# Kernel tuning notes

Measured on AMD Instinct MI355X. Metric: run time of the kernel, lower is better.

The kernel has to match this reference:

```python
import jax, jax.numpy as jnp
import numpy as np

N = 50000
E = 800000
F_IN = 128
HEADS = 8
HID = 16
CLASSES = 40
NEG_SLOPE = 0.2


def setup_inputs() -> dict:
    key = jax.random.key(0)
    ks = jax.random.split(key, 10)
    return {
        "x": jax.random.normal(ks[0], (N, F_IN), jnp.float32),
        "edge_index": jax.random.randint(ks[1], (2, E), 0, N, jnp.int64),
        "W1": jax.random.normal(ks[2], (F_IN, HEADS * HID), jnp.float32) * 0.1,
        "a_src1": jax.random.normal(ks[3], (HEADS, HID), jnp.float32) * 0.1,
        "a_dst1": jax.random.normal(ks[4], (HEADS, HID), jnp.float32) * 0.1,
        "b1": jax.random.normal(ks[5], (HEADS * HID,), jnp.float32) * 0.1,
        "W2": jax.random.normal(ks[6], (HEADS * HID, CLASSES), jnp.float32) * 0.1,
        "a_src2": jax.random.normal(ks[7], (1, CLASSES), jnp.float32) * 0.1,
        "a_dst2": jax.random.normal(ks[8], (1, CLASSES), jnp.float32) * 0.1,
        "b2": jax.random.normal(ks[9], (CLASSES,), jnp.float32) * 0.1,
    }


def gat_conv(x, src, dst, W, a_src, a_dst, bias, heads, out_ch, concat):
    # x: [N, in] -> h: [N, H, C]
    h = (x @ W).reshape(N, heads, out_ch)
    e_src = jnp.einsum("nhc,hc->nh", h, a_src)  # [N, H]
    e_dst = jnp.einsum("nhc,hc->nh", h, a_dst)
    alpha = e_src[src] + e_dst[dst]             # [E, H]
    alpha = jax.nn.leaky_relu(alpha, NEG_SLOPE)
    # segment softmax over incoming edges of each dst node
    amax = jax.ops.segment_max(alpha, dst, num_segments=N)
    alpha = jnp.exp(alpha - amax[dst])
    denom = jax.ops.segment_sum(alpha, dst, num_segments=N)
    alpha = alpha / (denom[dst] + 1e-16)
    msg = h[src] * alpha[:, :, None]            # [E, H, C]
    out = jax.ops.segment_sum(msg, dst, num_segments=N)  # [N, H, C]
    out = out.reshape(N, heads * out_ch) if concat else out.mean(axis=1)
    return out + bias


def reference(x, edge_index, W1, a_src1, a_dst1, b1, W2, a_src2, a_dst2, b2):
    # PyG GATConv adds self-loops by default
    loops = jnp.arange(N, dtype=edge_index.dtype)
    src = jnp.concatenate([edge_index[0], loops])
    dst = jnp.concatenate([edge_index[1], loops])
    # inference: dropout layers are identity
    h = gat_conv(x, src, dst, W1, a_src1, a_dst1, b1, HEADS, HID, concat=True)
    h = jax.nn.elu(h)
    out = gat_conv(h, src, dst, W2, a_src2, a_dst2, b2, 1, CLASSES, concat=False)
    return out
```

## Files before the change

kernel.cpp:

```cpp
#include <hip/hip_runtime.h>
#include <math.h>

#define NN 50000
#define EE 800000
#define ET (EE + NN)
#define F_IN 128
#define HEADS 8
#define HID 16
#define C1 (HEADS * HID)
#define CLASSES 40
#define NEG_SLOPE 0.2f
#define LOG2E 1.4426950408889634f

#define NCHUNKS ((NN + 1023) / 1024)
#define NHIST 64
#define EPB (EE / NHIST)
#define PADN (NCHUNKS * 1024)
#define LDSW (PADN / 4)
#define GB ((NN + 63) / 64)

typedef __attribute__((ext_vector_type(8))) short bf16x8;
typedef __attribute__((ext_vector_type(4))) float f32x4;
typedef __attribute__((ext_vector_type(8))) _Float16 h16x8;
typedef __attribute__((ext_vector_type(2))) _Float16 h16x2;

__device__ __forceinline__ unsigned cvtpk(float a, float b) {
    unsigned r;
    asm("v_cvt_pk_bf16_f32 %0, %1, %2" : "=v"(r) : "v"(a), "v"(b));
    return r;
}
__device__ __forceinline__ float fexp2(float x) {
    float r;
    asm("v_exp_f32 %0, %1\n\ts_nop 0" : "=v"(r) : "v"(x));
    return r;
}
__device__ __forceinline__ float bflo(unsigned u) { return __uint_as_float(u << 16); }
__device__ __forceinline__ float bfhi(unsigned u) { return __uint_as_float(u & 0xffff0000u); }
__device__ __forceinline__ float lrelu(float a) { return fmaxf(a, NEG_SLOPE * a); }
__device__ __forceinline__ unsigned short bf1(float a) { return (unsigned short)cvtpk(a, a); }
__device__ __forceinline__ float bf1f(float a) { return bflo(cvtpk(a, a)); }
__device__ __forceinline__ bf16x8 pack8(float f0, float f1, float f2, float f3,
                                        float f4, float f5, float f6, float f7) {
    union { unsigned u[4]; bf16x8 v; } U;
    U.u[0] = cvtpk(f0, f1);
    U.u[1] = cvtpk(f2, f3);
    U.u[2] = cvtpk(f4, f5);
    U.u[3] = cvtpk(f6, f7);
    return U.v;
}

__global__ void prep_kernel(const float* __restrict__ W1,
                            const float* __restrict__ as1, const float* __restrict__ ad1,
                            const float* __restrict__ W2,
                            const float* __restrict__ as2, const float* __restrict__ ad2,
                            const int* __restrict__ ei,
                            unsigned short* __restrict__ va1h, unsigned short* __restrict__ va1l,
                            unsigned short* __restrict__ va2b,
                            unsigned short* __restrict__ W1b, unsigned short* __restrict__ W2b,
                            unsigned char* __restrict__ partial8,
                            unsigned char* __restrict__ rank8) {
    const int tid = threadIdx.x;
    const int b = blockIdx.x;
    if (b >= 3) {
        __shared__ unsigned lhist[LDSW];
        for (int i = tid; i < LDSW; i += 256) lhist[i] = 0;
        __syncthreads();
        const int hb = b - 3;
        const int* dp = ei + EE + hb * EPB;
        unsigned char* rk = rank8 + (size_t)hb * EPB;
        for (int e0 = tid * 4; e0 < EPB; e0 += 1024) {
            int4 d4 = *(const int4*)(dp + e0);
            uchar4 r;
            {
                const unsigned d = (unsigned)d4.x, sh8 = (d & 3) << 3;
                unsigned old = atomicAdd(&lhist[d >> 2], 1u << sh8);
                r.x = (unsigned char)((old >> sh8) & 0xff);
            }
            {
                const unsigned d = (unsigned)d4.y, sh8 = (d & 3) << 3;
                unsigned old = atomicAdd(&lhist[d >> 2], 1u << sh8);
                r.y = (unsigned char)((old >> sh8) & 0xff);
            }
            {
                const unsigned d = (unsigned)d4.z, sh8 = (d & 3) << 3;
                unsigned old = atomicAdd(&lhist[d >> 2], 1u << sh8);
                r.z = (unsigned char)((old >> sh8) & 0xff);
            }
            {
                const unsigned d = (unsigned)d4.w, sh8 = (d & 3) << 3;
                unsigned old = atomicAdd(&lhist[d >> 2], 1u << sh8);
                r.w = (unsigned char)((old >> sh8) & 0xff);
            }
            *(uchar4*)(rk + e0) = r;
        }
        __syncthreads();
        unsigned* pb = (unsigned*)(partial8 + (size_t)hb * PADN);
        for (int i = tid; i < LDSW; i += 256) pb[i] = lhist[i];
        return;
    }
    if (b == 1) {
        for (int f = tid; f < 2048; f += 256) {
            const int lane = f & 63, kc = (f >> 6) & 3, ntw = f >> 8;
            const int q = lane >> 4, c = lane & 15;
            const int col = ntw * 16 + c;
            const int k0 = kc * 32 + q * 8;
            const float* wp = W1 + (size_t)k0 * C1 + col;
            *(bf16x8*)(W1b + (size_t)f * 8) =
                pack8(wp[0], wp[C1], wp[2 * C1], wp[3 * C1],
                      wp[4 * C1], wp[5 * C1], wp[6 * C1], wp[7 * C1]);
        }
        return;
    }
    if (b == 2) {
        for (int f = tid; f < 768; f += 256) {
            const int lane = f & 63, kc = (f >> 6) & 3, nt = f >> 8;
            const int q = lane >> 4, c = lane & 15;
            const int col = nt * 16 + c;
            const int k0 = kc * 32 + q * 8;
            bf16x8 v = 0;
            if (col < CLASSES) {
                const float* wp = W2 + (size_t)k0 * CLASSES + col;
                v = pack8(wp[0], wp[CLASSES], wp[2 * CLASSES], wp[3 * CLASSES],
                          wp[4 * CLASSES], wp[5 * CLASSES], wp[6 * CLASSES], wp[7 * CLASSES]);
            }
            *(bf16x8*)(W2b + (size_t)f * 8) = v;
        }
        return;
    }
    {
        const int k = tid >> 1, half = tid & 1;
        const float* wrow = W1 + (size_t)k * C1 + half * 64;
        #pragma unroll
        for (int hh = 0; hh < 4; ++hh) {
            const int h = half * 4 + hh;
            float s = 0.f, d = 0.f;
            #pragma unroll
            for (int t = 0; t < 16; ++t) {
                float wv = wrow[hh * 16 + t];
                s += wv * as1[h * HID + t];
                d += wv * ad1[h * HID + t];
            }
            s *= LOG2E; d *= LOG2E;
            va1h[h * 128 + k]       = bf1(s);
            va1l[h * 128 + k]       = bf1(s - bf1f(s));
            va1h[(h + 8) * 128 + k] = bf1(d);
            va1l[(h + 8) * 128 + k] = bf1(d - bf1f(d));
        }
    }
    if (tid < C1) {
        const float* wrow = W2 + (size_t)tid * CLASSES;
        float s = 0.f, d = 0.f;
        #pragma unroll
        for (int c2 = 0; c2 < CLASSES; ++c2) {
            float wv = wrow[c2];
            s += wv * as2[c2];
            d += wv * ad2[c2];
        }
        s *= LOG2E; d *= LOG2E;
        va2b[0 * 128 + tid] = bf1(s);
        va2b[1 * 128 + tid] = bf1(s - bf1f(s));
        va2b[2 * 128 + tid] = bf1(d);
        va2b[3 * 128 + tid] = bf1(d - bf1f(d));
    }
}

__global__ void scan1_kernel(const unsigned char* __restrict__ partial8,
                             unsigned char* __restrict__ pfx8,
                             int* __restrict__ deg,
                             int* __restrict__ rowptr, int* __restrict__ bsum) {
    __shared__ int sh[256];
    const int tid = threadIdx.x;
    const int base = blockIdx.x * 1024 + tid * 4;
    int t0 = 0, t1 = 0, t2 = 0, t3 = 0;
    #pragma unroll 8
    for (int b = 0; b < NHIST; ++b) {
        uchar4 pf;
        pf.x = (unsigned char)t0; pf.y = (unsigned char)t1;
        pf.z = (unsigned char)t2; pf.w = (unsigned char)t3;
        *(uchar4*)(pfx8 + (size_t)b * PADN + base) = pf;
        uchar4 p = *(const uchar4*)(partial8 + (size_t)b * PADN + base);
        t0 += p.x; t1 += p.y; t2 += p.z; t3 += p.w;
    }
    int v[4], s[4];
    v[0] = (base + 0 < NN) ? t0 + 1 : 0;
    v[1] = (base + 1 < NN) ? t1 + 1 : 0;
    v[2] = (base + 2 < NN) ? t2 + 1 : 0;
    v[3] = (base + 3 < NN) ? t3 + 1 : 0;
    #pragma unroll
    for (int j = 0; j < 4; ++j)
        if (base + j < NN) deg[base + j] = v[j];
    s[0] = v[0]; s[1] = s[0] + v[1]; s[2] = s[1] + v[2]; s[3] = s[2] + v[3];
    int T = s[3];
    sh[tid] = T;
    __syncthreads();
    for (int off = 1; off < 256; off <<= 1) {
        int xv = (tid >= off) ? sh[tid - off] : 0;
        __syncthreads();
        sh[tid] += xv;
        __syncthreads();
    }
    int excl = sh[tid] - T;
    #pragma unroll
    for (int j = 0; j < 4; ++j)
        if (base + j < NN) rowptr[base + j] = excl + s[j] - v[j];
    if (tid == 255) bsum[blockIdx.x] = sh[255];
}

__global__ void scan3_kernel(int* __restrict__ rowptr, const int* __restrict__ bsum,
                             unsigned short* __restrict__ csr) {
    __shared__ int ex[64];
    const int tid = threadIdx.x;
    if (tid < 64) {
        int v = (tid < NCHUNKS) ? bsum[tid] : 0;
        int s = v;
        #pragma unroll
        for (int off = 1; off < 64; off <<= 1) {
            int xv = __shfl_up(s, off);
            if (tid >= off) s += xv;
        }
        ex[tid] = s - v;
    }
    __syncthreads();
    int i = blockIdx.x * blockDim.x + tid;
    if (i >= NN) return;
    int rp = rowptr[i] + ex[i >> 10];
    rowptr[i] = rp;
    csr[rp] = (unsigned short)i;
}

__global__ __launch_bounds__(256, 4)
void gemm1_fill_kernel(const float* __restrict__ x,
                       const unsigned short* __restrict__ W1b,
                       const unsigned short* __restrict__ va1h,
                       const unsigned short* __restrict__ va1l,
                       const int* __restrict__ ei,
                       const int* __restrict__ rowptr,
                       const unsigned char* __restrict__ pfx8,
                       const unsigned char* __restrict__ rank8,
                       unsigned short* __restrict__ csr,
                       _Float16* __restrict__ h1h,
                       float* __restrict__ e_src, float* __restrict__ e_dst) {
    const int bid = blockIdx.x;
    const int tid = threadIdx.x;
    if (bid < NHIST) {
        const int fb = bid;
        const int* sp = ei + fb * EPB;
        const int* dp = ei + EE + fb * EPB;
        const unsigned char* pf = pfx8 + (size_t)fb * PADN;
        const unsigned char* rk = rank8 + (size_t)fb * EPB;
        for (int e0 = tid * 4; e0 < EPB; e0 += 1024) {
            int4 s4 = *(const int4*)(sp + e0);
            int4 d4 = *(const int4*)(dp + e0);
            uchar4 r = *(const uchar4*)(rk + e0);
            csr[rowptr[d4.x] + 1 + pf[d4.x] + r.x] = (unsigned short)s4.x;
            csr[rowptr[d4.y] + 1 + pf[d4.y] + r.y] = (unsigned short)s4.y;
            csr[rowptr[d4.z] + 1 + pf[d4.z] + r.z] = (unsigned short)s4.z;
            csr[rowptr[d4.w] + 1 + pf[d4.w] + r.w] = (unsigned short)s4.w;
        }
        return;
    }
    const int gemmb = bid - NHIST;
    const int w = tid >> 6, lane = tid & 63;
    const int q = lane >> 4, c = lane & 15;
    const int m0 = (gemmb * 4 + w) * 16;

    int row = m0 + c;
    if (row > NN - 1) row = NN - 1;
    bf16x8 afrag[4];
    #pragma unroll
    for (int kc = 0; kc < 4; ++kc) {
        const float* xp = x + (size_t)row * F_IN + kc * 32 + q * 8;
        float4 p0 = *(const float4*)xp;
        float4 p1 = *(const float4*)(xp + 4);
        afrag[kc] = pack8(p0.x, p0.y, p0.z, p0.w, p1.x, p1.y, p1.z, p1.w);
    }

    {
        f32x4 acce = {0.f, 0.f, 0.f, 0.f};
        #pragma unroll
        for (int kc = 0; kc < 4; ++kc) {
            const int coloff = kc * 32 + q * 8;
            bf16x8 beh = *(const bf16x8*)(va1h + c * 128 + coloff);
            bf16x8 bel = *(const bf16x8*)(va1l + c * 128 + coloff);
            acce = __builtin_amdgcn_mfma_f32_16x16x32_bf16(afrag[kc], beh, acce, 0, 0, 0);
            acce = __builtin_amdgcn_mfma_f32_16x16x32_bf16(afrag[kc], bel, acce, 0, 0, 0);
        }
        float* ep = (c < 8) ? e_src : e_dst;
        const int cc = c & 7;
        #pragma unroll
        for (int r = 0; r < 4; ++r) {
            const int ro = m0 + q * 4 + r;
            if (ro < NN) ep[(size_t)ro * HEADS + cc] = acce[r];
        }
    }

    #pragma unroll 2
    for (int nt = 0; nt < 8; ++nt) {
        bf16x8 bf0 = *(const bf16x8*)(W1b + (size_t)((nt * 4 + 0) * 64 + lane) * 8);
        bf16x8 bf1_ = *(const bf16x8*)(W1b + (size_t)((nt * 4 + 1) * 64 + lane) * 8);
        bf16x8 bf2 = *(const bf16x8*)(W1b + (size_t)((nt * 4 + 2) * 64 + lane) * 8);
        bf16x8 bf3 = *(const bf16x8*)(W1b + (size_t)((nt * 4 + 3) * 64 + lane) * 8);
        f32x4 a = {0.f, 0.f, 0.f, 0.f};
        a = __builtin_amdgcn_mfma_f32_16x16x32_bf16(afrag[0], bf0, a, 0, 0, 0);
        a = __builtin_amdgcn_mfma_f32_16x16x32_bf16(afrag[1], bf1_, a, 0, 0, 0);
        a = __builtin_amdgcn_mfma_f32_16x16x32_bf16(afrag[2], bf2, a, 0, 0, 0);
        a = __builtin_amdgcn_mfma_f32_16x16x32_bf16(afrag[3], bf3, a, 0, 0, 0);
        #pragma unroll
        for (int r = 0; r < 4; ++r) {
            const int ro = m0 + q * 4 + r;
            if (ro < NN) h1h[(size_t)ro * C1 + nt * 16 + c] = (_Float16)a[r];
        }
    }
}

__global__ __launch_bounds__(64)
void agg1_kernel(const _Float16* __restrict__ h1h,
                 const float* __restrict__ e_src, const float* __restrict__ e_dst,
                 const int* __restrict__ rowptr, const int* __restrict__ deg,
                 const unsigned short* __restrict__ csr,
                 const float* __restrict__ b1, unsigned short* __restrict__ hmid) {
    const int tid = threadIdx.x;
    const int l = tid & 15;
    const int d = blockIdx.x * 4 + (tid >> 4);
    const int hd = l >> 1;
    const float ed = e_dst[(size_t)d * HEADS + hd];
    const int start = rowptr[d];
    const int cnt = deg[d];

    float denom = 0.f;
    float acc[8] = {0.f, 0.f, 0.f, 0.f, 0.f, 0.f, 0.f, 0.f};

    for (int i = 0; i < cnt; i += 8) {
        int s[8];
        #pragma unroll
        for (int e = 0; e < 8; ++e)
            s[e] = csr[start + ((i + e < cnt) ? i + e : i)];
        float es[8];
        #pragma unroll
        for (int e = 0; e < 8; ++e)
            es[e] = e_src[(size_t)s[e] * HEADS + hd];
        h16x8 g[8];
        #pragma unroll
        for (int e = 0; e < 8; ++e)
            g[e] = *(const h16x8*)(h1h + (size_t)s[e] * C1 + 8 * l);
        float w[8];
        #pragma unroll
        for (int e = 0; e < 8; ++e) {
            float we = fexp2(lrelu(es[e] + ed));
            w[e] = (i + e < cnt) ? we : 0.f;
            denom += w[e];
        }
        #pragma unroll
        for (int e = 0; e < 8; ++e) {
            #pragma unroll
            for (int j = 0; j < 8; ++j)
                acc[j] = fmaf((float)g[e][j], w[e], acc[j]);
        }
    }
    const float inv = 1.f / (denom + 1e-16f);
    float o[8];
    #pragma unroll
    for (int k = 0; k < 8; ++k) {
        float t = acc[k] * inv + b1[8 * l + k];
        o[k] = (t > 0.f) ? t : fexp2(t * LOG2E) - 1.f;
    }
    uint4 st;
    st.x = cvtpk(o[0], o[1]);
    st.y = cvtpk(o[2], o[3]);
    st.z = cvtpk(o[4], o[5]);
    st.w = cvtpk(o[6], o[7]);
    *(uint4*)(hmid + (size_t)d * C1 + 8 * l) = st;
}

__global__ __launch_bounds__(256, 4)
void gemm2_kernel(const unsigned short* __restrict__ hmid,
                  const unsigned short* __restrict__ W2b,
                  const unsigned short* __restrict__ va2b,
                  _Float16* __restrict__ h2h,
                  float* __restrict__ e_src, float* __restrict__ e_dst) {
    const int tid = threadIdx.x;
    const int w = tid >> 6, lane = tid & 63;
    const int q = lane >> 4, c = lane & 15;

    const int m0 = (blockIdx.x * 4 + w) * 16;
    if (m0 >= NN) return;
    int row = m0 + c;
    if (row > NN - 1) row = NN - 1;
    bf16x8 afrag[4];
    #pragma unroll
    for (int kc = 0; kc < 4; ++kc)
        afrag[kc] = *(const bf16x8*)(hmid + (size_t)row * C1 + kc * 32 + q * 8);

    bf16x8 bfrag[3][4];
    #pragma unroll
    for (int nt = 0; nt < 3; ++nt)
        #pragma unroll
        for (int kc = 0; kc < 4; ++kc)
            bfrag[nt][kc] = *(const bf16x8*)(W2b + (size_t)((nt * 4 + kc) * 64 + lane) * 8);
    bf16x8 bfe[4];
    #pragma unroll
    for (int kc = 0; kc < 4; ++kc) {
        bf16x8 bb = 0;
        if (c < 4) bb = *(const bf16x8*)(va2b + c * 128 + kc * 32 + q * 8);
        bfe[kc] = bb;
    }

    f32x4 acc[3] = {{0.f,0.f,0.f,0.f},{0.f,0.f,0.f,0.f},{0.f,0.f,0.f,0.f}};
    f32x4 acce = {0.f, 0.f, 0.f, 0.f};
    #pragma unroll
    for (int kc = 0; kc < 4; ++kc) {
        acc[0] = __builtin_amdgcn_mfma_f32_16x16x32_bf16(afrag[kc], bfrag[0][kc], acc[0], 0, 0, 0);
        acc[1] = __builtin_amdgcn_mfma_f32_16x16x32_bf16(afrag[kc], bfrag[1][kc], acc[1], 0, 0, 0);
        acc[2] = __builtin_amdgcn_mfma_f32_16x16x32_bf16(afrag[kc], bfrag[2][kc], acc[2], 0, 0, 0);
        acce   = __builtin_amdgcn_mfma_f32_16x16x32_bf16(afrag[kc], bfe[kc],      acce,   0, 0, 0);
    }
    #pragma unroll
    for (int r = 0; r < 4; ++r) {
        const int ro = m0 + q * 4 + r;
        float v = acce[r] + __shfl_xor(acce[r], 1);
        if (ro < NN) {
            #pragma unroll
            for (int nt = 0; nt < 3; ++nt) {
                const int col = nt * 16 + c;
                if (col < CLASSES)
                    h2h[(size_t)ro * CLASSES + col] = (_Float16)acc[nt][r];
            }
            if (c == 0) e_src[ro] = v;
            if (c == 2) e_dst[ro] = v;
        }
    }
}

__global__ __launch_bounds__(64)
void agg2_kernel(const _Float16* __restrict__ h2h,
                 const float* __restrict__ e_src, const float* __restrict__ e_dst,
                 const int* __restrict__ rowptr, const int* __restrict__ deg,
                 const unsigned short* __restrict__ csr,
                 const float* __restrict__ b2, float* __restrict__ out) {
    const int tid = threadIdx.x;
    const int eg = tid / 20;
    const int c  = tid % 20;
    const int d = blockIdx.x * 3 + eg;
    const bool live = (eg < 3) && (d < NN);
    const int dcl = live ? d : 0;
    const float ed = e_dst[dcl];
    const int start = rowptr[dcl];
    const int cnt = live ? deg[dcl] : 0;

    float denom = 0.f, acc0 = 0.f, acc1 = 0.f;
    for (int i = 0; i < cnt; i += 8) {
        int s[8];
        #pragma unroll
        for (int e = 0; e < 8; ++e)
            s[e] = csr[start + ((i + e < cnt) ? i + e : i)];
        float es[8];
        #pragma unroll
        for (int e = 0; e < 8; ++e)
            es[e] = e_src[s[e]];
        h16x2 g[8];
        #pragma unroll
        for (int e = 0; e < 8; ++e)
            g[e] = *(const h16x2*)(h2h + (size_t)s[e] * CLASSES + 2 * c);
        float w[8];
        #pragma unroll
        for (int e = 0; e < 8; ++e) {
            float we = fexp2(lrelu(es[e] + ed));
            w[e] = (i + e < cnt) ? we : 0.f;
            denom += w[e];
        }
        #pragma unroll
        for (int e = 0; e < 8; ++e) {
            acc0 = fmaf((float)g[e][0], w[e], acc0);
            acc1 = fmaf((float)g[e][1], w[e], acc1);
        }
    }
    if (live) {
        const float inv = 1.f / (denom + 1e-16f);
        float2 o;
        o.x = acc0 * inv + b2[2 * c];
        o.y = acc1 * inv + b2[2 * c + 1];
        *(float2*)(out + (size_t)d * CLASSES + 2 * c) = o;
    }
}

extern "C" void kernel_launch(void* const* d_in, const int* in_sizes, int n_in,
                              void* d_out, int out_size, void* d_ws, size_t ws_size,
                              hipStream_t stream) {
    const float* x      = (const float*)d_in[0];
    const int*   ei     = (const int*)d_in[1];
    const float* W1     = (const float*)d_in[2];
    const float* a_src1 = (const float*)d_in[3];
    const float* a_dst1 = (const float*)d_in[4];
    const float* b1     = (const float*)d_in[5];
    const float* W2     = (const float*)d_in[6];
    const float* a_src2 = (const float*)d_in[7];
    const float* a_dst2 = (const float*)d_in[8];
    const float* b2     = (const float*)d_in[9];
    float* out = (float*)d_out;

    char* ws = (char*)d_ws;
    size_t off = 0;
    auto alloc = [&](size_t bytes) { char* p = ws + off; off += (bytes + 255) & ~(size_t)255; return p; };
    _Float16* h1h = (_Float16*)alloc((size_t)NN * C1 * 2);
    _Float16* h2h = (_Float16*)alloc((size_t)NN * CLASSES * 2);
    unsigned short* hmidb = (unsigned short*)alloc((size_t)NN * C1 * 2);
    float* e_src1 = (float*)alloc((size_t)NN * HEADS * 4);
    float* e_dst1 = (float*)alloc((size_t)NN * HEADS * 4);
    float* e_src2 = (float*)alloc((size_t)NN * 4);
    float* e_dst2 = (float*)alloc((size_t)NN * 4);
    int*   deg    = (int*)alloc((size_t)NN * 4);
    int*   rowptr = (int*)alloc((size_t)NN * 4);
    unsigned short* csr  = (unsigned short*)alloc((size_t)ET * 2);
    int*   bsum   = (int*)alloc(256 * 4);
    unsigned short* va1h = (unsigned short*)alloc(16 * 128 * 2);
    unsigned short* va1l = (unsigned short*)alloc(16 * 128 * 2);
    unsigned short* va2b = (unsigned short*)alloc(4 * 128 * 2);
    unsigned short* W1b  = (unsigned short*)alloc(2048 * 8 * 2);
    unsigned short* W2b  = (unsigned short*)alloc(768 * 8 * 2);
    unsigned char* partial8 = (unsigned char*)alloc((size_t)NHIST * PADN);
    unsigned char* pfx8     = (unsigned char*)alloc((size_t)NHIST * PADN);
    unsigned char* rank8    = (unsigned char*)alloc((size_t)EE);

    prep_kernel<<<3 + NHIST, 256, 0, stream>>>(W1, a_src1, a_dst1, W2, a_src2, a_dst2, ei,
                                               va1h, va1l, va2b, W1b, W2b, partial8, rank8);
    scan1_kernel<<<NCHUNKS, 256, 0, stream>>>(partial8, pfx8, deg, rowptr, bsum);
    scan3_kernel<<<(NN + 255) / 256, 256, 0, stream>>>(rowptr, bsum, csr);
    gemm1_fill_kernel<<<NHIST + GB, 256, 0, stream>>>(x, W1b, va1h, va1l, ei, rowptr, pfx8,
                                                      rank8, csr, h1h, e_src1, e_dst1);

    agg1_kernel<<<NN / 4, 64, 0, stream>>>(h1h, e_src1, e_dst1, rowptr, deg, csr, b1, hmidb);

    gemm2_kernel<<<(NN + 63) / 64, 256, 0, stream>>>(hmidb, W2b, va2b, h2h, e_src2, e_dst2);
    agg2_kernel<<<(NN + 2) / 3, 64, 0, stream>>>(h2h, e_src2, e_dst2, rowptr, deg, csr, b2, out);
}
```

Before: 206.4 us.

## Fuse layer-1 aggregation with layer-2 GEMM and split CSR fill across more blocks

Layer-1 aggregation now writes each block's 16 output rows into shared memory, and one wave then runs the layer-2 MFMA GEMM on them directly. This drops the hmid buffer round-trip through global memory and one kernel launch. Separately, the CSR fill phase is split into five sub-blocks per histogram partition so more blocks share the scatter work. In exchange, three of the four waves sit idle during the fused GEMM phase, and the blocks are larger (256 threads covering 16 nodes), which may change load balance across nodes of different degree.

```diff
diff --git a/kernel.cpp b/kernel.cpp
--- a/kernel.cpp
+++ b/kernel.cpp
@@ -18,6 +18,9 @@
 #define PADN (NCHUNKS * 1024)
 #define LDSW (PADN / 4)
 #define GB ((NN + 63) / 64)
+#define FSUB 5
+#define FPB (EPB / FSUB)
+#define FILLB (NHIST * FSUB)
 
 typedef __attribute__((ext_vector_type(8))) short bf16x8;
 typedef __attribute__((ext_vector_type(4))) float f32x4;
@@ -242,13 +245,15 @@
                        float* __restrict__ e_src, float* __restrict__ e_dst) {
     const int bid = blockIdx.x;
     const int tid = threadIdx.x;
-    if (bid < NHIST) {
-        const int fb = bid;
-        const int* sp = ei + fb * EPB;
-        const int* dp = ei + EE + fb * EPB;
-        const unsigned char* pf = pfx8 + (size_t)fb * PADN;
-        const unsigned char* rk = rank8 + (size_t)fb * EPB;
-        for (int e0 = tid * 4; e0 < EPB; e0 += 1024) {
+    if (bid < FILLB) {
+        const int part = bid / FSUB;
+        const int chunkoff = (bid % FSUB) * FPB;
+        const int gbase = part * EPB + chunkoff;
+        const int* sp = ei + gbase;
+        const int* dp = ei + EE + gbase;
+        const unsigned char* pf = pfx8 + (size_t)part * PADN;
+        const unsigned char* rk = rank8 + (size_t)part * EPB + chunkoff;
+        for (int e0 = tid * 4; e0 < FPB; e0 += 1024) {
             int4 s4 = *(const int4*)(sp + e0);
             int4 d4 = *(const int4*)(dp + e0);
             uchar4 r = *(const uchar4*)(rk + e0);
@@ -259,7 +264,7 @@
         }
         return;
     }
-    const int gemmb = bid - NHIST;
+    const int gemmb = bid - FILLB;
     const int w = tid >> 6, lane = tid & 63;
     const int q = lane >> 4, c = lane & 15;
     const int m0 = (gemmb * 4 + w) * 16;
@@ -313,15 +318,21 @@
     }
 }
 
-__global__ __launch_bounds__(64)
-void agg1_kernel(const _Float16* __restrict__ h1h,
-                 const float* __restrict__ e_src, const float* __restrict__ e_dst,
-                 const int* __restrict__ rowptr, const int* __restrict__ deg,
-                 const unsigned short* __restrict__ csr,
-                 const float* __restrict__ b1, unsigned short* __restrict__ hmid) {
+__global__ __launch_bounds__(256)
+void agg1_gemm2_kernel(const _Float16* __restrict__ h1h,
+                       const float* __restrict__ e_src, const float* __restrict__ e_dst,
+                       const int* __restrict__ rowptr, const int* __restrict__ deg,
+                       const unsigned short* __restrict__ csr,
+                       const float* __restrict__ b1,
+                       const unsigned short* __restrict__ W2b,
+                       const unsigned short* __restrict__ va2b,
+                       _Float16* __restrict__ h2h,
+                       float* __restrict__ e_src2, float* __restrict__ e_dst2) {
+    __shared__ unsigned short hm[16][132];
     const int tid = threadIdx.x;
+    const int grp = tid >> 4;
     const int l = tid & 15;
-    const int d = blockIdx.x * 4 + (tid >> 4);
+    const int d = blockIdx.x * 16 + grp;
     const int hd = l >> 1;
     const float ed = e_dst[(size_t)d * HEADS + hd];
     const int start = rowptr[d];
@@ -369,64 +380,52 @@
     st.y = cvtpk(o[2], o[3]);
     st.z = cvtpk(o[4], o[5]);
     st.w = cvtpk(o[6], o[7]);
-    *(uint4*)(hmid + (size_t)d * C1 + 8 * l) = st;
-}
-
-__global__ __launch_bounds__(256, 4)
-void gemm2_kernel(const unsigned short* __restrict__ hmid,
-                  const unsigned short* __restrict__ W2b,
-                  const unsigned short* __restrict__ va2b,
-                  _Float16* __restrict__ h2h,
-                  float* __restrict__ e_src, float* __restrict__ e_dst) {
-    const int tid = threadIdx.x;
-    const int w = tid >> 6, lane = tid & 63;
-    const int q = lane >> 4, c = lane & 15;
-
-    const int m0 = (blockIdx.x * 4 + w) * 16;
-    if (m0 >= NN) return;
-    int row = m0 + c;
-    if (row > NN - 1) row = NN - 1;
-    bf16x8 afrag[4];
-    #pragma unroll
-    for (int kc = 0; kc < 4; ++kc)
-        afrag[kc] = *(const bf16x8*)(hmid + (size_t)row * C1 + kc * 32 + q * 8);
-
-    bf16x8 bfrag[3][4];
-    #pragma unroll
-    for (int nt = 0; nt < 3; ++nt)
+    *(uint4*)(&hm[grp][8 * l]) = st;
+    __syncthreads();
+
+    if (tid < 64) {
+        const int lane = tid, q = lane >> 4, c = lane & 15;
+        const int m0 = blockIdx.x * 16;
+        bf16x8 afrag[4];
         #pragma unroll
         for (int kc = 0; kc < 4; ++kc)
-            bfrag[nt][kc] = *(const bf16x8*)(W2b + (size_t)((nt * 4 + kc) * 64 + lane) * 8);
-    bf16x8 bfe[4];
-    #pragma unroll
-    for (int kc = 0; kc < 4; ++kc) {
-        bf16x8 bb = 0;
-        if (c < 4) bb = *(const bf16x8*)(va2b + c * 128 + kc * 32 + q * 8);
-        bfe[kc] = bb;
-    }
-
-    f32x4 acc[3] = {{0.f,0.f,0.f,0.f},{0.f,0.f,0.f,0.f},{0.f,0.f,0.f,0.f}};
-    f32x4 acce = {0.f, 0.f, 0.f, 0.f};
-    #pragma unroll
-    for (int kc = 0; kc < 4; ++kc) {
-        acc[0] = __builtin_amdgcn_mfma_f32_16x16x32_bf16(afrag[kc], bfrag[0][kc], acc[0], 0, 0, 0);
-        acc[1] = __builtin_amdgcn_mfma_f32_16x16x32_bf16(afrag[kc], bfrag[1][kc], acc[1], 0, 0, 0);
-        acc[2] = __builtin_amdgcn_mfma_f32_16x16x32_bf16(afrag[kc], bfrag[2][kc], acc[2], 0, 0, 0);
-        acce   = __builtin_amdgcn_mfma_f32_16x16x32_bf16(afrag[kc], bfe[kc],      acce,   0, 0, 0);
-    }
-    #pragma unroll
-    for (int r = 0; r < 4; ++r) {
-        const int ro = m0 + q * 4 + r;
-        float v = acce[r] + __shfl_xor(acce[r], 1);
-        if (ro < NN) {
+            afrag[kc] = *(const bf16x8*)(&hm[c][kc * 32 + q * 8]);
+
+        bf16x8 bfrag[3][4];
+        #pragma unroll
+        for (int nt = 0; nt < 3; ++nt)
+            #pragma unroll
+            for (int kc = 0; kc < 4; ++kc)
+                bfrag[nt][kc] = *(const bf16x8*)(W2b + (size_t)((nt * 4 + kc) * 64 + lane) * 8);
+        bf16x8 bfe[4];
+        #pragma unroll
+        for (int kc = 0; kc < 4; ++kc) {
+            bf16x8 bb = 0;
+            if (c < 4) bb = *(const bf16x8*)(va2b + c * 128 + kc * 32 + q * 8);
+            bfe[kc] = bb;
+        }
+
+        f32x4 a2[3] = {{0.f,0.f,0.f,0.f},{0.f,0.f,0.f,0.f},{0.f,0.f,0.f,0.f}};
+        f32x4 acce = {0.f, 0.f, 0.f, 0.f};
+        #pragma unroll
+        for (int kc = 0; kc < 4; ++kc) {
+            a2[0] = __builtin_amdgcn_mfma_f32_16x16x32_bf16(afrag[kc], bfrag[0][kc], a2[0], 0, 0, 0);
+            a2[1] = __builtin_amdgcn_mfma_f32_16x16x32_bf16(afrag[kc], bfrag[1][kc], a2[1], 0, 0, 0);
+            a2[2] = __builtin_amdgcn_mfma_f32_16x16x32_bf16(afrag[kc], bfrag[2][kc], a2[2], 0, 0, 0);
+            acce  = __builtin_amdgcn_mfma_f32_16x16x32_bf16(afrag[kc], bfe[kc],      acce,  0, 0, 0);
+        }
+        #pragma unroll
+        for (int r = 0; r < 4; ++r) {
+            const int ro = m0 + q * 4 + r;
+            float v = acce[r] + __shfl_xor(acce[r], 1);
             #pragma unroll
             for (int nt = 0; nt < 3; ++nt) {
                 const int col = nt * 16 + c;
                 if (col < CLASSES)
-                    h2h[(size_t)ro * CLASSES + col] = (_Float16)acc[nt][r];
-            }
-            if (c == 0) e_src[ro] = v;
-            if (c == 2) e_dst[ro] = v;
+                    h2h[(size_t)ro * CLASSES + col] = (_Float16)a2[nt][r];
+            }
+            if (c == 0) e_src2[ro] = v;
+            if (c == 2) e_dst2[ro] = v;
         }
     }
 }
@@ -503,7 +502,6 @@
     auto alloc = [&](size_t bytes) { char* p = ws + off; off += (bytes + 255) & ~(size_t)255; return p; };
     _Float16* h1h = (_Float16*)alloc((size_t)NN * C1 * 2);
     _Float16* h2h = (_Float16*)alloc((size_t)NN * CLASSES * 2);
-    unsigned short* hmidb = (unsigned short*)alloc((size_t)NN * C1 * 2);
     float* e_src1 = (float*)alloc((size_t)NN * HEADS * 4);
     float* e_dst1 = (float*)alloc((size_t)NN * HEADS * 4);
     float* e_src2 = (float*)alloc((size_t)NN * 4);
@@ -525,11 +523,11 @@
                                                va1h, va1l, va2b, W1b, W2b, partial8, rank8);
     scan1_kernel<<<NCHUNKS, 256, 0, stream>>>(partial8, pfx8, deg, rowptr, bsum);
     scan3_kernel<<<(NN + 255) / 256, 256, 0, stream>>>(rowptr, bsum, csr);
-    gemm1_fill_kernel<<<NHIST + GB, 256, 0, stream>>>(x, W1b, va1h, va1l, ei, rowptr, pfx8,
+    gemm1_fill_kernel<<<FILLB + GB, 256, 0, stream>>>(x, W1b, va1h, va1l, ei, rowptr, pfx8,
                                                       rank8, csr, h1h, e_src1, e_dst1);
 
-    agg1_kernel<<<NN / 4, 64, 0, stream>>>(h1h, e_src1, e_dst1, rowptr, deg, csr, b1, hmidb);
-
-    gemm2_kernel<<<(NN + 63) / 64, 256, 0, stream>>>(hmidb, W2b, va2b, h2h, e_src2, e_dst2);
+    agg1_gemm2_kernel<<<NN / 16, 256, 0, stream>>>(h1h, e_src1, e_dst1, rowptr, deg, csr, b1,
+                                                   W2b, va2b, h2h, e_src2, e_dst2);
+
     agg2_kernel<<<(NN + 2) / 3, 64, 0, stream>>>(h2h, e_src2, e_dst2, rowptr, deg, csr, b2, out);
 }
```

New measurement: 196.0 us. 5.0% less time.
